# Performance work log

Measured on AMD Instinct MI355X. Metric: run time of the kernel, lower is better.

The kernel has to match this reference:

```python
import jax, jax.numpy as jnp
import numpy as np

B, N, D = 4, 2048, 512
H = 8            # num_heads (even)
HE = H // 2      # effective heads = 4
DH = D // H      # head_dim = 64
LAMBDA_INIT = 0.8
EPS = 1e-5


def setup_inputs() -> dict:
    key = jax.random.key(0)
    ks = jax.random.split(key, 10)
    return {
        "q": jax.random.normal(ks[0], (B, N, D), jnp.float32),
        "k": jax.random.normal(ks[1], (B, N, D), jnp.float32),
        "v": jax.random.normal(ks[2], (B, N, D), jnp.float32),
        "lambda_q1": 0.1 * jax.random.normal(ks[3], (DH,), jnp.float32),
        "lambda_k1": 0.1 * jax.random.normal(ks[4], (DH,), jnp.float32),
        "lambda_q2": 0.1 * jax.random.normal(ks[5], (DH,), jnp.float32),
        "lambda_k2": 0.1 * jax.random.normal(ks[6], (DH,), jnp.float32),
        "norm_w": jnp.ones((2 * DH,), jnp.float32),
        "out_w": 0.02 * jax.random.normal(ks[7], (D, D), jnp.float32),  # torch Linear weight [out,in]
        "out_b": jnp.zeros((D,), jnp.float32),
    }


def reference(q, k, v, lambda_q1, lambda_k1, lambda_q2, lambda_k2, norm_w, out_w, out_b):
    b, nq, d = q.shape
    nk = k.shape[1]
    # split heads: q,k -> [B, 2*HE, N, DH]; v -> [B, HE, Nk, 2*DH]
    qh = q.reshape(b, nq, 2 * HE, DH).transpose(0, 2, 1, 3) * (DH ** -0.5)
    kh = k.reshape(b, nk, 2 * HE, DH).transpose(0, 2, 1, 3)
    vh = v.reshape(b, nk, HE, 2 * DH).transpose(0, 2, 1, 3)
    scores = jnp.einsum('bhqd,bhkd->bhqk', qh, kh)          # [B, 2HE, Nq, Nk]
    probs = jax.nn.softmax(scores, axis=-1)
    probs = probs.reshape(b, HE, 2, nq, nk)
    lam = (jnp.exp(jnp.sum(lambda_q1 * lambda_k1))
           - jnp.exp(jnp.sum(lambda_q2 * lambda_k2)) + LAMBDA_INIT)
    diff = probs[:, :, 0] - lam * probs[:, :, 1]            # [B, HE, Nq, Nk]
    out = jnp.einsum('bhqk,bhkd->bhqd', diff, vh)           # [B, HE, Nq, 2*DH]
    # per-head RMSNorm over last dim (2*DH), elementwise affine
    out = out * jax.lax.rsqrt(jnp.mean(out * out, axis=-1, keepdims=True) + EPS)
    out = out * norm_w * (1.0 - LAMBDA_INIT)
    out = out.transpose(0, 2, 1, 3).reshape(b, nq, d)
    return out @ out_w.T + out_b
```

## Files before the change

### kernel.cpp

```cpp
#include <hip/hip_runtime.h>
#include <math.h>

#define BB 4
#define NN 2048
#define DD 512
#define LAMBDA_INIT 0.8f
#define EPSV 1e-5f

typedef __attribute__((ext_vector_type(8))) short bf16x8;
typedef __attribute__((ext_vector_type(4))) float f32x4;
typedef __attribute__((ext_vector_type(16))) float f32x16;
typedef unsigned short u16;
typedef __attribute__((ext_vector_type(4))) u16 u16x4;
typedef __attribute__((ext_vector_type(8))) u16 u16x8;
typedef __attribute__((ext_vector_type(4))) unsigned u32x4;

__device__ __forceinline__ u16 f2bf(float f) {
  unsigned u = __builtin_bit_cast(unsigned, f);
  u = (u + 0x7FFFu + ((u >> 16) & 1u)) >> 16;
  return (u16)u;
}

__device__ __forceinline__ void gload16(const void* g, void* l) {
  __builtin_amdgcn_global_load_lds((const __attribute__((address_space(1))) unsigned*)g,
                                   (__attribute__((address_space(3))) unsigned*)l, 16, 0, 0);
}

__device__ __forceinline__ f32x16 fz16() {
  f32x16 z;
  #pragma unroll
  for (int i = 0; i < 16; ++i) z[i] = 0.f;
  return z;
}

__device__ __forceinline__ void plswap(unsigned &a, unsigned &b) {
  asm("v_permlane32_swap_b32 %0, %1" : "+v"(a), "+v"(b));
}
__device__ __forceinline__ float xhalf_add(float x) {
  unsigned a = __builtin_bit_cast(unsigned, x), b;
  asm("v_mov_b32 %0, %1" : "=v"(b) : "v"(a));
  asm("v_permlane32_swap_b32 %0, %1" : "+v"(a), "+v"(b));
  return __builtin_bit_cast(float, a) + __builtin_bit_cast(float, b);
}

__global__ __launch_bounds__(256) void prep_kernel(
    const float* __restrict__ q, const float* __restrict__ k, const float* __restrict__ w,
    u16* __restrict__ Qb, u16* __restrict__ Kb, u16* __restrict__ Wb)
{
  const int t = threadIdx.x;
  const int bid = blockIdx.x;
  if (bid >= BB * NN) {
    const size_t idx = (size_t)(bid - BB * NN) * 256 + t;
    float4 f = *(const float4*)&w[idx * 4];
    u16x4 o = { f2bf(f.x), f2bf(f.y), f2bf(f.z), f2bf(f.w) };
    *(u16x4*)&Wb[idx * 4] = o;
    return;
  }
  const size_t row = bid;
  const int n = bid & (NN - 1);
  const int b = bid >> 11;
  if (t < 128) {
    const float s = 0.125f * 1.4426950408889634f;
    float4 f = *(const float4*)&q[row * DD + t * 4];
    u16x4 o = { f2bf(f.x * s), f2bf(f.y * s), f2bf(f.z * s), f2bf(f.w * s) };
    *(u16x4*)&Qb[row * DD + t * 4] = o;
  } else {
    const int f0 = (t - 128) * 4;
    float4 f = *(const float4*)&k[row * DD + f0];
    const int he = f0 >> 7, fi = f0 & 127;
    const int gi = fi >> 3, lo = fi & 7;
    const int gi2 = (gi & 8) | ((gi & 7) ^ (n & 7));
    u16x4 o = { f2bf(f.x), f2bf(f.y), f2bf(f.z), f2bf(f.w) };
    *(u16x4*)&Kb[((size_t)(b * 4 + he) * NN + n) * 128 + gi2 * 8 + lo] = o;
  }
}

__global__ __launch_bounds__(256) void v_prep_kernel(const float* __restrict__ v, u16* __restrict__ Vbt) {
  __shared__ u16 Ls[64][72];
  const int t = threadIdx.x;
  const int n0 = blockIdx.x * 64;
  const int d0 = blockIdx.y * 64;
  const int z  = blockIdx.z;
  #pragma unroll
  for (int p = 0; p < 4; ++p) {
    int n = p * 16 + (t >> 4), f4 = t & 15;
    float4 rv = *(const float4*)&v[((size_t)((z >> 2) * NN + n0 + n)) * DD + (z & 3) * 128 + d0 + f4 * 4];
    Ls[n][f4*4+0] = f2bf(rv.x); Ls[n][f4*4+1] = f2bf(rv.y);
    Ls[n][f4*4+2] = f2bf(rv.z); Ls[n][f4*4+3] = f2bf(rv.w);
  }
  __syncthreads();
  #pragma unroll
  for (int rep = 0; rep < 2; ++rep) {
    const int sid   = rep * 256 + t;
    const int tt    = sid >> 8;
    const int rem   = sid & 255;
    const int i_rel = rem >> 6;
    const int ls    = rem & 63;
    const int i_    = (d0 >> 4) + i_rel;
    const int j     = i_ * 8 + (ls >> 3);
    const int s0    = (ls & 7) ^ (j & 7);
    const int dl    = 2 * (i_rel * 8 + (ls >> 3)) + (s0 >> 2);
    const int nl0   = tt * 32 + (s0 & 3) * 8;
    u16x8 o;
    #pragma unroll
    for (int jj = 0; jj < 8; ++jj) o[jj] = Ls[nl0 + jj][dl];
    const int tile = blockIdx.x * 2 + tt;
    *(u16x8*)&Vbt[((size_t)z * 64 + tile) * 4096 + i_ * 512 + ls * 8] = o;
  }
}

#define ISSUE_K8(dst, kv0) do { \
  _Pragma("unroll") for (int i_ = 0; i_ < 8; ++i_) \
    gload16(kgb + (((size_t)(kv0) + i_ * 4 + (l >> 4)) << 7) + ((l & 15) << 3), (dst) + i_ * 512); \
  __builtin_amdgcn_sched_barrier(0); } while (0)

#define ISSUE_V8(dst, kv0) do { \
  _Pragma("unroll") for (int i_ = 0; i_ < 8; ++i_) \
    gload16(vgb + ((size_t)((kv0) >> 5)) * 4096 + i_ * 512 + l * 8, (dst) + i_ * 512); \
  __builtin_amdgcn_sched_barrier(0); } while (0)

#define WAIT_VM0 do { asm volatile("s_waitcnt vmcnt(0)" ::: "memory"); \
  __builtin_amdgcn_sched_barrier(0); } while (0)

__global__ __launch_bounds__(256, 2) void attn8_kernel(
    const u16* __restrict__ Qb, const u16* __restrict__ Kb, const u16* __restrict__ Vbt,
    const float* __restrict__ lq1, const float* __restrict__ lk1,
    const float* __restrict__ lq2, const float* __restrict__ lk2,
    const float* __restrict__ norm_w, u16* __restrict__ Xb)
{
  __shared__ __align__(16) u16 smem[32768];
  __shared__ float stats[2][2][2][32];

  u16* KB = smem;
  u16* VB = smem + 16384;

  const int tid = threadIdx.x;
  const int w   = tid >> 6;
  const int l   = tid & 63;
  const int hi  = l >> 5;
  const int q   = l & 31;
  const int h   = w >> 1;
  const int kvh = w & 1;

  const int bid0 = blockIdx.x;
  const int bid = (bid0 & 7) * 64 + (bid0 >> 3);
  const int qt = bid & 31;
  const int he = (bid >> 5) & 3;
  const int b  = bid >> 7;
  const int q0 = qt * 64;
  const int bhe = b * 4 + he;

  float lp1 = lq1[l] * lk1[l], lp2 = lq2[l] * lk2[l];
  #pragma unroll
  for (int off = 32; off; off >>= 1) { lp1 += __shfl_xor(lp1, off); lp2 += __shfl_xor(lp2, off); }
  const float lam = __expf(lp1) - __expf(lp2) + LAMBDA_INIT;
  asm volatile("" :: "v"(lam));

  bf16x8 qf[2][4];
  #pragma unroll
  for (int g = 0; g < 2; ++g) {
    const u16* qp = Qb + ((size_t)(b * NN) + q0 + g * 32 + q) * DD + he * 128 + h * 64 + hi * 8;
    #pragma unroll
    for (int dk = 0; dk < 4; ++dk)
      qf[g][dk] = *(const bf16x8*)(qp + dk * 16);
  }
  WAIT_VM0;
  #pragma unroll
  for (int g = 0; g < 2; ++g)
    #pragma unroll
    for (int dk = 0; dk < 4; ++dk)
      asm volatile("" :: "v"(qf[g][dk]));

  const u16* kgb = Kb + (size_t)bhe * NN * 128;
  const u16* vgb = Vbt + (size_t)bhe * 64 * 4096;
  const int kvb = kvh * 1024;

  if (h == 0) ISSUE_K8(&KB[kvh * 8192], kvb);
  else        ISSUE_V8(&VB[kvh * 8192], kvb);

  f32x16 O[2][4];
  #pragma unroll
  for (int g = 0; g < 2; ++g)
    #pragma unroll
    for (int dt = 0; dt < 4; ++dt) O[g][dt] = fz16();
  float sl[2] = {0.f, 0.f};

  const int jq  = (q >> 1) & 7;
  const int dq1 = (q & 1) << 2;

  for (int tt = 0; tt < 32; ++tt) {
    WAIT_VM0;
    __builtin_amdgcn_s_barrier();
    __builtin_amdgcn_sched_barrier(0);

    {
      const int kvn = kvb + ((tt + 1) & 31) * 32;
      const int db = (tt + 1) & 1;
      if (h == 0) ISSUE_K8(&KB[(kvh * 2 + db) * 4096], kvn);
      else        ISSUE_V8(&VB[(kvh * 2 + db) * 4096], kvn);
    }

    const u16* Kcur = &KB[(kvh * 2 + (tt & 1)) * 4096];
    const u16* Vcur = &VB[(kvh * 2 + (tt & 1)) * 4096];

    f32x16 Sg[2];
    __builtin_amdgcn_s_setprio(1);
    {
      f32x16 a0 = fz16(), a1 = fz16();
      #pragma unroll
      for (int dk = 0; dk < 4; ++dk) {
        const int gd = h * 8 + dk * 2 + hi;
        const int g2 = (gd & 8) | ((gd & 7) ^ (q & 7));
        bf16x8 kf = *(const bf16x8*)&Kcur[q * 128 + g2 * 8];
        a0 = __builtin_amdgcn_mfma_f32_32x32x16_bf16(kf, qf[0][dk], a0, 0, 0, 0);
        a1 = __builtin_amdgcn_mfma_f32_32x32x16_bf16(kf, qf[1][dk], a1, 0, 0, 0);
      }
      Sg[0] = a0; Sg[1] = a1;
    }
    __builtin_amdgcn_s_setprio(0);

    bf16x8 pb[2][2];
    #pragma unroll
    for (int g = 0; g < 2; ++g) {
      #pragma unroll
      for (int r = 0; r < 16; ++r)
        Sg[g][r] = __builtin_amdgcn_exp2f(Sg[g][r]);
      {
        float y0 = (Sg[g][0]  + Sg[g][1])  + (Sg[g][2]  + Sg[g][3]);
        float y1 = (Sg[g][4]  + Sg[g][5])  + (Sg[g][6]  + Sg[g][7]);
        float y2 = (Sg[g][8]  + Sg[g][9])  + (Sg[g][10] + Sg[g][11]);
        float y3 = (Sg[g][12] + Sg[g][13]) + (Sg[g][14] + Sg[g][15]);
        sl[g] += (y0 + y1) + (y2 + y3);
      }
      unsigned PK[8];
      #pragma unroll
      for (int p2 = 0; p2 < 8; ++p2)
        asm("v_cvt_pk_bf16_f32 %0, %1, %2" : "=v"(PK[p2]) : "v"(Sg[g][2*p2]), "v"(Sg[g][2*p2+1]));
      #pragma unroll
      for (int kb = 0; kb < 2; ++kb) {
        unsigned w0 = PK[4*kb + 0], w2v = PK[4*kb + 2];
        unsigned w1 = PK[4*kb + 1], w3v = PK[4*kb + 3];
        plswap(w0, w2v);
        plswap(w1, w3v);
        union { u32x4 u; bf16x8 v; } cv;
        cv.u = (u32x4){ w0, w1, w2v, w3v };
        pb[g][kb] = cv.v;
      }
    }

    __builtin_amdgcn_s_setprio(1);
    #pragma unroll
    for (int kk = 0; kk < 2; ++kk)
      #pragma unroll
      for (int dt = 0; dt < 4; ++dt) {
        const int j = dt * 16 + (q >> 1);
        const int s8 = (dq1 + kk * 2 + hi) ^ jq;
        bf16x8 vf = *(const bf16x8*)&Vcur[j * 64 + s8 * 8];
        O[0][dt] = __builtin_amdgcn_mfma_f32_32x32x16_bf16(vf, pb[0][kk], O[0][dt], 0, 0, 0);
        O[1][dt] = __builtin_amdgcn_mfma_f32_32x32x16_bf16(vf, pb[1][kk], O[1][dt], 0, 0, 0);
      }
    __builtin_amdgcn_s_setprio(0);
  }

  WAIT_VM0;
  __syncthreads();

  #pragma unroll
  for (int g = 0; g < 2; ++g) sl[g] = xhalf_add(sl[g]);
  if (hi == 0) { stats[h][kvh][0][q] = sl[0]; stats[h][kvh][1][q] = sl[1]; }
  __syncthreads();
  float L[2];
  #pragma unroll
  for (int g = 0; g < 2; ++g) L[g] = stats[h][0][g][q] + stats[h][1][g][q];

  float* xch = (float*)smem;
  if (kvh == 1) {
    #pragma unroll
    for (int g = 0; g < 2; ++g)
      #pragma unroll
      for (int dt = 0; dt < 4; ++dt)
        #pragma unroll
        for (int r = 0; r < 16; ++r) {
          const int crow = (r & 3) + 8 * (r >> 2) + 4 * hi;
          xch[h * 8192 + (dt * 32 + crow) * 64 + g * 32 + q] = O[g][dt][r];
        }
  }
  __syncthreads();
  if (kvh == 0) {
    #pragma unroll
    for (int g = 0; g < 2; ++g)
      #pragma unroll
      for (int dt = 0; dt < 4; ++dt)
        #pragma unroll
        for (int r = 0; r < 16; ++r) {
          const int crow = (r & 3) + 8 * (r >> 2) + 4 * hi;
          O[g][dt][r] += xch[h * 8192 + (dt * 32 + crow) * 64 + g * 32 + q];
        }
  }
  __syncthreads();
  if (kvh == 0 && h == 1) {
    #pragma unroll
    for (int g = 0; g < 2; ++g) {
      const float s2 = lam / L[g];
      #pragma unroll
      for (int dt = 0; dt < 4; ++dt)
        #pragma unroll
        for (int r = 0; r < 16; ++r) {
          const int crow = (r & 3) + 8 * (r >> 2) + 4 * hi;
          xch[(dt * 32 + crow) * 64 + g * 32 + q] = O[g][dt][r] * s2;
        }
    }
  }
  __syncthreads();
  if (kvh == 0 && h == 0) {
    #pragma unroll
    for (int g = 0; g < 2; ++g) {
      const float i1 = 1.f / L[g];
      float ss = 0.f;
      #pragma unroll
      for (int dt = 0; dt < 4; ++dt)
        #pragma unroll
        for (int r = 0; r < 16; ++r) {
          const int crow = (r & 3) + 8 * (r >> 2) + 4 * hi;
          float o = O[g][dt][r] * i1 - xch[(dt * 32 + crow) * 64 + g * 32 + q];
          O[g][dt][r] = o;
          ss += o * o;
        }
      ss = xhalf_add(ss);
      const float rstd = rsqrtf(ss * (1.f / 128.f) + EPSV);
      const size_t xo = ((size_t)(b * NN) + q0 + g * 32 + q) * DD + he * 128;
      #pragma unroll
      for (int dt = 0; dt < 4; ++dt)
        #pragma unroll
        for (int rq = 0; rq < 4; ++rq) {
          const int d0 = dt * 32 + rq * 8 + hi * 4;
          const float4 nw = *(const float4*)&norm_w[d0];
          u16x4 ov;
          ov[0] = f2bf(O[g][dt][rq*4 + 0] * rstd * nw.x * 0.2f);
          ov[1] = f2bf(O[g][dt][rq*4 + 1] * rstd * nw.y * 0.2f);
          ov[2] = f2bf(O[g][dt][rq*4 + 2] * rstd * nw.z * 0.2f);
          ov[3] = f2bf(O[g][dt][rq*4 + 3] * rstd * nw.w * 0.2f);
          *(u16x4*)&Xb[xo + d0] = ov;
        }
    }
  }
}

#define PLOAD(k0) do { \
    _Pragma("unroll") for (int p_ = 0; p_ < 2; ++p_) { \
      int idx_ = p_*256 + t; int r_ = idx_ >> 3, gi_ = idx_ & 7; \
      ra[p_] = *(const u16x8*)&Xb[(size_t)(row0 + r_) * DD + (k0) + gi_*8]; \
      rb[p_] = *(const u16x8*)&Wb[(size_t)(col0 + r_) * DD + (k0) + gi_*8]; } \
  } while (0)
#define PWRITE(bi) do { \
    _Pragma("unroll") for (int p_ = 0; p_ < 2; ++p_) { \
      int idx_ = p_*256 + t; int r_ = idx_ >> 3, gi_ = idx_ & 7; \
      *(u16x8*)&As[bi][r_*64 + ((gi_ ^ (r_ & 7)) << 3)] = ra[p_]; \
      *(u16x8*)&Bs[bi][r_*64 + ((gi_ ^ (r_ & 7)) << 3)] = rb[p_]; } \
  } while (0)

__global__ __launch_bounds__(256, 2) void proj_mfma_kernel(
    const u16* __restrict__ Xb, const u16* __restrict__ Wb,
    const float* __restrict__ bias, float* __restrict__ out)
{
  __shared__ __align__(16) u16 As[2][64*64];
  __shared__ __align__(16) u16 Bs[2][64*64];
  const int t = threadIdx.x;
  const int w = t >> 6, l = t & 63, g = l >> 4, c = l & 15;
  const int wm = w >> 1, wn = w & 1;
  const int row0 = blockIdx.x * 64, col0 = blockIdx.y * 64;

  u16x8 ra[2], rb[2];
  f32x4 acc[2][2];
  #pragma unroll
  for (int i = 0; i < 2; ++i)
    #pragma unroll
    for (int j = 0; j < 2; ++j) acc[i][j] = (f32x4){0,0,0,0};
  float bj[2];
  #pragma unroll
  for (int j = 0; j < 2; ++j) bj[j] = bias[col0 + wn*32 + j*16 + c];

  PLOAD(0);
  PWRITE(0);
  __syncthreads();
  for (int s = 0; s < 8; ++s) {
    const int bi = s & 1;
    if (s < 7) PLOAD((s + 1) * 64);
    #pragma unroll
    for (int kc = 0; kc < 2; ++kc) {
      bf16x8 af[2], bfv[2];
      #pragma unroll
      for (int i = 0; i < 2; ++i) {
        int rowa = wm*32 + i*16 + c;
        af[i]  = *(const bf16x8*)&As[bi][rowa*64 + (((kc*4 + g) ^ (c & 7)) << 3)];
        int rowb = wn*32 + i*16 + c;
        bfv[i] = *(const bf16x8*)&Bs[bi][rowb*64 + (((kc*4 + g) ^ (c & 7)) << 3)];
      }
      #pragma unroll
      for (int i = 0; i < 2; ++i)
        #pragma unroll
        for (int j = 0; j < 2; ++j)
          acc[i][j] = __builtin_amdgcn_mfma_f32_16x16x32_bf16(af[i], bfv[j], acc[i][j], 0, 0, 0);
    }
    if (s < 7) PWRITE((s + 1) & 1);
    __syncthreads();
  }
  #pragma unroll
  for (int i = 0; i < 2; ++i)
    #pragma unroll
    for (int j = 0; j < 2; ++j)
      #pragma unroll
      for (int rr = 0; rr < 4; ++rr)
        out[(size_t)(row0 + wm*32 + i*16 + g*4 + rr) * DD + col0 + wn*32 + j*16 + c] = acc[i][j][rr] + bj[j];
}

extern "C" void kernel_launch(void* const* d_in, const int* in_sizes, int n_in,
                              void* d_out, int out_size, void* d_ws, size_t ws_size,
                              hipStream_t stream) {
    const float* q      = (const float*)d_in[0];
    const float* k      = (const float*)d_in[1];
    const float* v      = (const float*)d_in[2];
    const float* lq1    = (const float*)d_in[3];
    const float* lk1    = (const float*)d_in[4];
    const float* lq2    = (const float*)d_in[5];
    const float* lk2    = (const float*)d_in[6];
    const float* norm_w = (const float*)d_in[7];
    const float* out_w  = (const float*)d_in[8];
    const float* out_b  = (const float*)d_in[9];
    float* out = (float*)d_out;

    u16* Qb  = (u16*)d_ws;
    u16* Kb  = (u16*)((char*)d_ws + (8u  << 20));
    u16* Vbt = (u16*)((char*)d_ws + (16u << 20));
    u16* Wb  = (u16*)((char*)d_ws + (24u << 20));
    u16* Xb  = (u16*)((char*)d_ws + (25u << 20));

    prep_kernel<<<BB * NN + 256, 256, 0, stream>>>(q, k, out_w, Qb, Kb, Wb);
    v_prep_kernel<<<dim3(32, 2, 16), 256, 0, stream>>>(v, Vbt);
    attn8_kernel<<<512, 256, 0, stream>>>(Qb, Kb, Vbt, lq1, lk1, lq2, lk2, norm_w, Xb);
    proj_mfma_kernel<<<dim3(128, 8), 256, 0, stream>>>(Xb, Wb, out_b, out);
}
```

Baseline: 96.53 us.

## Split attention blocks by query group instead of KV half, with 4-stage K/V ring

Each block now covers 128 query rows, and its two wave pairs split them into query groups; before, the pairs split the KV sequence. All waves share each K/V tile, so each loaded tile is reused across twice as many queries and the cross-wave partial-sum merge and stats exchange go away. The K/V loads become a 4-slot ring with three tiles in flight, waited on with vmcnt(8), replacing the double buffer. The trade-off is half as many blocks (256), which may leave compute units underfilled, and a longer serial loop of 64 tiles per block.

After: 99.08 us. 1.03x slower.

```diff
diff --git a/kernel.cpp b/kernel.cpp
--- a/kernel.cpp
+++ b/kernel.cpp
@@ -109,30 +109,28 @@
   }
 }
 
-#define ISSUE_K8(dst, kv0) do { \
-  _Pragma("unroll") for (int i_ = 0; i_ < 8; ++i_) \
-    gload16(kgb + (((size_t)(kv0) + i_ * 4 + (l >> 4)) << 7) + ((l & 15) << 3), (dst) + i_ * 512); \
+#define ISSUE_K4(dst, kv0, part) do { \
+  _Pragma("unroll") for (int i_ = 0; i_ < 4; ++i_) { int ii_ = (part)*4 + i_; \
+    gload16(kgb + (((size_t)(kv0) + ii_ * 4 + (l >> 4)) << 7) + ((l & 15) << 3), (dst) + ii_ * 512); } \
   __builtin_amdgcn_sched_barrier(0); } while (0)
 
-#define ISSUE_V8(dst, kv0) do { \
-  _Pragma("unroll") for (int i_ = 0; i_ < 8; ++i_) \
-    gload16(vgb + ((size_t)((kv0) >> 5)) * 4096 + i_ * 512 + l * 8, (dst) + i_ * 512); \
+#define ISSUE_V4(dst, kv0, part) do { \
+  _Pragma("unroll") for (int i_ = 0; i_ < 4; ++i_) { int ii_ = (part)*4 + i_; \
+    gload16(vgb + ((size_t)((kv0) >> 5)) * 4096 + ii_ * 512 + l * 8, (dst) + ii_ * 512); } \
   __builtin_amdgcn_sched_barrier(0); } while (0)
 
+#define WAIT_VM(n) do { asm volatile("s_waitcnt vmcnt(" #n ")" ::: "memory"); \
+  __builtin_amdgcn_sched_barrier(0); } while (0)
 #define WAIT_VM0 do { asm volatile("s_waitcnt vmcnt(0)" ::: "memory"); \
   __builtin_amdgcn_sched_barrier(0); } while (0)
 
-__global__ __launch_bounds__(256, 2) void attn8_kernel(
+__global__ __launch_bounds__(256, 2) void attn9_kernel(
     const u16* __restrict__ Qb, const u16* __restrict__ Kb, const u16* __restrict__ Vbt,
     const float* __restrict__ lq1, const float* __restrict__ lk1,
     const float* __restrict__ lq2, const float* __restrict__ lk2,
     const float* __restrict__ norm_w, u16* __restrict__ Xb)
 {
   __shared__ __align__(16) u16 smem[32768];
-  __shared__ float stats[2][2][2][32];
-
-  u16* KB = smem;
-  u16* VB = smem + 16384;
 
   const int tid = threadIdx.x;
   const int w   = tid >> 6;
@@ -140,14 +138,14 @@
   const int hi  = l >> 5;
   const int q   = l & 31;
   const int h   = w >> 1;
-  const int kvh = w & 1;
+  const int qg  = w & 1;
 
   const int bid0 = blockIdx.x;
-  const int bid = (bid0 & 7) * 64 + (bid0 >> 3);
-  const int qt = bid & 31;
-  const int he = (bid >> 5) & 3;
-  const int b  = bid >> 7;
-  const int q0 = qt * 64;
+  const int bid = (bid0 & 7) * 32 + (bid0 >> 3);
+  const int qt = bid & 15;
+  const int he = (bid >> 4) & 3;
+  const int b  = bid >> 6;
+  const int q0 = qt * 128;
   const int bhe = b * 4 + he;
 
   float lp1 = lq1[l] * lk1[l], lp2 = lq2[l] * lk2[l];
@@ -159,7 +157,7 @@
   bf16x8 qf[2][4];
   #pragma unroll
   for (int g = 0; g < 2; ++g) {
-    const u16* qp = Qb + ((size_t)(b * NN) + q0 + g * 32 + q) * DD + he * 128 + h * 64 + hi * 8;
+    const u16* qp = Qb + ((size_t)(b * NN) + q0 + qg * 64 + g * 32 + q) * DD + he * 128 + h * 64 + hi * 8;
     #pragma unroll
     for (int dk = 0; dk < 4; ++dk)
       qf[g][dk] = *(const bf16x8*)(qp + dk * 16);
@@ -173,10 +171,13 @@
 
   const u16* kgb = Kb + (size_t)bhe * NN * 128;
   const u16* vgb = Vbt + (size_t)bhe * 64 * 4096;
-  const int kvb = kvh * 1024;
-
-  if (h == 0) ISSUE_K8(&KB[kvh * 8192], kvb);
-  else        ISSUE_V8(&VB[kvh * 8192], kvb);
+
+  #pragma unroll
+  for (int pt = 0; pt < 3; ++pt) {
+    u16* slot = smem + pt * 8192;
+    if (h == 0) ISSUE_K4(slot, pt * 32, qg);
+    else        ISSUE_V4(slot + 4096, pt * 32, qg);
+  }
 
   f32x16 O[2][4];
   #pragma unroll
@@ -188,20 +189,20 @@
   const int jq  = (q >> 1) & 7;
   const int dq1 = (q & 1) << 2;
 
-  for (int tt = 0; tt < 32; ++tt) {
-    WAIT_VM0;
+  for (int tt = 0; tt < 64; ++tt) {
+    WAIT_VM(8);
     __builtin_amdgcn_s_barrier();
     __builtin_amdgcn_sched_barrier(0);
 
     {
-      const int kvn = kvb + ((tt + 1) & 31) * 32;
-      const int db = (tt + 1) & 1;
-      if (h == 0) ISSUE_K8(&KB[(kvh * 2 + db) * 4096], kvn);
-      else        ISSUE_V8(&VB[(kvh * 2 + db) * 4096], kvn);
-    }
-
-    const u16* Kcur = &KB[(kvh * 2 + (tt & 1)) * 4096];
-    const u16* Vcur = &VB[(kvh * 2 + (tt & 1)) * 4096];
+      const int nt = (tt + 3) & 63;
+      u16* slot = smem + ((tt + 3) & 3) * 8192;
+      if (h == 0) ISSUE_K4(slot, nt * 32, qg);
+      else        ISSUE_V4(slot + 4096, nt * 32, qg);
+    }
+
+    const u16* Kcur = smem + (tt & 3) * 8192;
+    const u16* Vcur = Kcur + 4096;
 
     f32x16 Sg[2];
     __builtin_amdgcn_s_setprio(1);
@@ -265,70 +266,42 @@
   WAIT_VM0;
   __syncthreads();
 
-  #pragma unroll
-  for (int g = 0; g < 2; ++g) sl[g] = xhalf_add(sl[g]);
-  if (hi == 0) { stats[h][kvh][0][q] = sl[0]; stats[h][kvh][1][q] = sl[1]; }
-  __syncthreads();
   float L[2];
   #pragma unroll
-  for (int g = 0; g < 2; ++g) L[g] = stats[h][0][g][q] + stats[h][1][g][q];
+  for (int g = 0; g < 2; ++g) L[g] = xhalf_add(sl[g]);
 
   float* xch = (float*)smem;
-  if (kvh == 1) {
-    #pragma unroll
-    for (int g = 0; g < 2; ++g)
+  if (h == 1) {
+    #pragma unroll
+    for (int g = 0; g < 2; ++g) {
+      const float s2 = lam / L[g];
       #pragma unroll
       for (int dt = 0; dt < 4; ++dt)
         #pragma unroll
         for (int r = 0; r < 16; ++r) {
           const int crow = (r & 3) + 8 * (r >> 2) + 4 * hi;
-          xch[h * 8192 + (dt * 32 + crow) * 64 + g * 32 + q] = O[g][dt][r];
+          xch[(dt * 32 + crow) * 128 + qg * 64 + g * 32 + q] = O[g][dt][r] * s2;
         }
+    }
   }
   __syncthreads();
-  if (kvh == 0) {
-    #pragma unroll
-    for (int g = 0; g < 2; ++g)
+  if (h == 0) {
+    #pragma unroll
+    for (int g = 0; g < 2; ++g) {
+      const float i1 = 1.f / L[g];
+      float ss = 0.f;
       #pragma unroll
       for (int dt = 0; dt < 4; ++dt)
         #pragma unroll
         for (int r = 0; r < 16; ++r) {
           const int crow = (r & 3) + 8 * (r >> 2) + 4 * hi;
-          O[g][dt][r] += xch[h * 8192 + (dt * 32 + crow) * 64 + g * 32 + q];
-        }
-  }
-  __syncthreads();
-  if (kvh == 0 && h == 1) {
-    #pragma unroll
-    for (int g = 0; g < 2; ++g) {
-      const float s2 = lam / L[g];
-      #pragma unroll
-      for (int dt = 0; dt < 4; ++dt)
-        #pragma unroll
-        for (int r = 0; r < 16; ++r) {
-          const int crow = (r & 3) + 8 * (r >> 2) + 4 * hi;
-          xch[(dt * 32 + crow) * 64 + g * 32 + q] = O[g][dt][r] * s2;
-        }
-    }
-  }
-  __syncthreads();
-  if (kvh == 0 && h == 0) {
-    #pragma unroll
-    for (int g = 0; g < 2; ++g) {
-      const float i1 = 1.f / L[g];
-      float ss = 0.f;
-      #pragma unroll
-      for (int dt = 0; dt < 4; ++dt)
-        #pragma unroll
-        for (int r = 0; r < 16; ++r) {
-          const int crow = (r & 3) + 8 * (r >> 2) + 4 * hi;
-          float o = O[g][dt][r] * i1 - xch[(dt * 32 + crow) * 64 + g * 32 + q];
+          float o = O[g][dt][r] * i1 - xch[(dt * 32 + crow) * 128 + qg * 64 + g * 32 + q];
           O[g][dt][r] = o;
           ss += o * o;
         }
       ss = xhalf_add(ss);
       const float rstd = rsqrtf(ss * (1.f / 128.f) + EPSV);
-      const size_t xo = ((size_t)(b * NN) + q0 + g * 32 + q) * DD + he * 128;
+      const size_t xo = ((size_t)(b * NN) + q0 + qg * 64 + g * 32 + q) * DD + he * 128;
       #pragma unroll
       for (int dt = 0; dt < 4; ++dt)
         #pragma unroll
@@ -437,6 +410,6 @@
 
     prep_kernel<<<BB * NN + 256, 256, 0, stream>>>(q, k, out_w, Qb, Kb, Wb);
     v_prep_kernel<<<dim3(32, 2, 16), 256, 0, stream>>>(v, Vbt);
-    attn8_kernel<<<512, 256, 0, stream>>>(Qb, Kb, Vbt, lq1, lk1, lq2, lk2, norm_w, Xb);
+    attn9_kernel<<<256, 256, 0, stream>>>(Qb, Kb, Vbt, lq1, lk1, lq2, lk2, norm_w, Xb);
     proj_mfma_kernel<<<dim3(128, 8), 256, 0, stream>>>(Xb, Wb, out_b, out);
 }
```
